# Optimization experiments

Hardware: AMD Instinct MI355X
Metric: run time of the kernel (lower is better)

The kernel has to match this reference:

```python
import jax, jax.numpy as jnp
import numpy as np

B, NQ, NM = 8, 1024, 2048
DIM, HEADS, DHEAD, MLP = 512, 8, 64, 2048
INNER = HEADS * DHEAD
EPS = 1e-5


def layernorm(x, g, b):
    mu = jnp.mean(x, axis=-1, keepdims=True)
    var = jnp.mean(jnp.square(x - mu), axis=-1, keepdims=True)
    return (x - mu) * jax.lax.rsqrt(var + EPS) * g + b


def mha(q_in, k_in, v_in, wq, wk, wv, wo, bo, g, b):
    Bq, Nq, _ = q_in.shape
    Nk = k_in.shape[1]
    q = (q_in @ wq).reshape(Bq, Nq, HEADS, DHEAD)
    k = (k_in @ wk).reshape(Bq, Nk, HEADS, DHEAD)
    v = (v_in @ wv).reshape(Bq, Nk, HEADS, DHEAD)
    scale = DHEAD ** -0.5
    dots = jnp.einsum('bqhd,bkhd->bhqk', q, k) * scale
    attn = jax.nn.softmax(dots, axis=-1)
    out = jnp.einsum('bhqk,bkhd->bqhd', attn, v).reshape(Bq, Nq, INNER)
    out = out @ wo + bo
    return layernorm(out, g, b) + q_in


def ffn(x, w1, b1, w2, b2, g, b):
    h = jax.nn.relu(x @ w1 + b1)
    return layernorm(h @ w2 + b2, g, b) + x


def _mha_params(key, s=0.02):
    ks = jax.random.split(key, 4)
    return dict(
        wq=jax.random.normal(ks[0], (DIM, INNER), jnp.float32) * s,
        wk=jax.random.normal(ks[1], (DIM, INNER), jnp.float32) * s,
        wv=jax.random.normal(ks[2], (DIM, INNER), jnp.float32) * s,
        wo=jax.random.normal(ks[3], (INNER, DIM), jnp.float32) * s,
        bo=jnp.zeros((DIM,), jnp.float32),
        g=jnp.ones((DIM,), jnp.float32),
        b=jnp.zeros((DIM,), jnp.float32),
    )


def _ffn_params(key, s=0.02):
    ks = jax.random.split(key, 2)
    return dict(
        w1=jax.random.normal(ks[0], (DIM, MLP), jnp.float32) * s,
        b1=jnp.zeros((MLP,), jnp.float32),
        w2=jax.random.normal(ks[1], (MLP, DIM), jnp.float32) * s,
        b2=jnp.zeros((DIM,), jnp.float32),
        g=jnp.ones((DIM,), jnp.float32),
        b=jnp.zeros((DIM,), jnp.float32),
    )


def setup_inputs() -> dict:
    key = jax.random.key(0)
    ks = jax.random.split(key, 8)
    inp = {
        'tgt': jax.random.normal(ks[0], (B, NQ, DIM), jnp.float32),
        'memory': jax.random.normal(ks[1], (B, NM, DIM), jnp.float32),
        'pos': jax.random.normal(ks[2], (B, NM, DIM), jnp.float32),
        'query_pos': jax.random.normal(ks[3], (B, NQ, DIM), jnp.float32),
    }
    a0 = _mha_params(ks[4]); f0 = _ffn_params(ks[5])
    a1 = _mha_params(ks[6]); f1 = _ffn_params(ks[7])
    for name, d in (('a0', a0), ('f0', f0), ('a1', a1), ('f1', f1)):
        for k, v in d.items():
            inp[f'{name}_{k}'] = v
    return inp


def reference(tgt, memory, pos, query_pos,
              a0_wq, a0_wk, a0_wv, a0_wo, a0_bo, a0_g, a0_b,
              f0_w1, f0_b1, f0_w2, f0_b2, f0_g, f0_b,
              a1_wq, a1_wk, a1_wv, a1_wo, a1_bo, a1_g, a1_b,
              f1_w1, f1_b1, f1_w2, f1_b2, f1_g, f1_b):
    # self-attention: q=k=tgt+query_pos, v=tgt
    q0 = tgt + query_pos
    x = mha(q0, q0, tgt, a0_wq, a0_wk, a0_wv, a0_wo, a0_bo, a0_g, a0_b)
    x = ffn(x, f0_w1, f0_b1, f0_w2, f0_b2, f0_g, f0_b)
    # cross-attention: q=x+query_pos, k=memory+pos, v=memory
    q = x + query_pos
    k = memory + pos
    x = mha(q, k, memory, a1_wq, a1_wk, a1_wv, a1_wo, a1_bo, a1_g, a1_b)
    x = ffn(x, f1_w1, f1_b1, f1_w2, f1_b2, f1_g, f1_b)
    return x
```

## Files before the change

### kernel.cpp

```cpp
#include <hip/hip_runtime.h>
#include <stdint.h>
#include <stddef.h>

typedef __attribute__((ext_vector_type(8))) short short8;
typedef __attribute__((ext_vector_type(4))) short short4v;
typedef __attribute__((ext_vector_type(4))) float floatx4;

#define DEV __device__ __forceinline__

DEV float bf2f(short s) {
    union { float f; uint32_t u; } v;
    v.u = ((uint32_t)(uint16_t)s) << 16;
    return v.f;
}
DEV short f2bf(float f) {
    union { float f; uint32_t u; } v;
    v.f = f;
    uint32_t u = v.u + 0x7FFFu + ((v.u >> 16) & 1u);
    return (short)(u >> 16);
}
DEV short f2bf_tr(float f) {
    union { float f; uint32_t u; } v;
    v.f = f;
    return (short)(v.u >> 16);
}

template<int BIAS, int RELU, int OUTBF>
__global__ __launch_bounds__(256) void gemm_bt(
    const short* __restrict__ A, const short* __restrict__ Bt,
    const float* __restrict__ bias, void* __restrict__ Cout,
    int M, int N, int K)
{
    __shared__ short Alds[2][128 * 32];
    __shared__ short Blds[2][128 * 32];
    const int tid  = threadIdx.x;
    const int wave = tid >> 6, lane = tid & 63;
    const int g = lane >> 4, li = lane & 15;

    const int gx = gridDim.x;
    int flat = blockIdx.y * gx + blockIdx.x;
    const int nwg = gx * gridDim.y;
    flat = (flat & 7) * (nwg >> 3) + (flat >> 3);
    const long bm = (long)(flat % gx) * 128;
    const long bn = (long)(flat / gx) * 128;

    const int wr = (wave >> 1) * 64;
    const int wc = (wave & 1) * 64;
    const int srow = wave * 32 + (lane >> 2);
    const int scol = (lane & 3) * 8;
    const short* Ap = A + bm * K + (long)srow * K + scol;
    const short* Bp = Bt + bn * K + (long)srow * K + scol;

    auto STAGE = [&](int buf, int k0) {
        __builtin_amdgcn_global_load_lds(
            (const __attribute__((address_space(1))) void*)(Ap + k0),
            (__attribute__((address_space(3))) void*)(&Alds[buf][wave * 1024]), 16, 0, 0);
        __builtin_amdgcn_global_load_lds(
            (const __attribute__((address_space(1))) void*)(Ap + (long)16 * K + k0),
            (__attribute__((address_space(3))) void*)(&Alds[buf][wave * 1024 + 512]), 16, 0, 0);
        __builtin_amdgcn_global_load_lds(
            (const __attribute__((address_space(1))) void*)(Bp + k0),
            (__attribute__((address_space(3))) void*)(&Blds[buf][wave * 1024]), 16, 0, 0);
        __builtin_amdgcn_global_load_lds(
            (const __attribute__((address_space(1))) void*)(Bp + (long)16 * K + k0),
            (__attribute__((address_space(3))) void*)(&Blds[buf][wave * 1024 + 512]), 16, 0, 0);
    };

    floatx4 acc[4][4];
#pragma unroll
    for (int i = 0; i < 4; i++)
#pragma unroll
        for (int j = 0; j < 4; j++) acc[i][j] = (floatx4){0.f, 0.f, 0.f, 0.f};

    STAGE(0, 0);
    __syncthreads();
    int cur = 0;
    for (int k0 = 0; k0 < K; k0 += 32) {
        if (k0 + 32 < K) STAGE(cur ^ 1, k0 + 32);

        short8 af[4], bfr[4];
#pragma unroll
        for (int mi = 0; mi < 4; mi++)
            af[mi] = *(const short8*)(&Alds[cur][(wr + mi * 16 + li) * 32 + g * 8]);
#pragma unroll
        for (int ni = 0; ni < 4; ni++)
            bfr[ni] = *(const short8*)(&Blds[cur][(wc + ni * 16 + li) * 32 + g * 8]);
#pragma unroll
        for (int mi = 0; mi < 4; mi++)
#pragma unroll
            for (int ni = 0; ni < 4; ni++)
                acc[mi][ni] = __builtin_amdgcn_mfma_f32_16x16x32_bf16(
                    af[mi], bfr[ni], acc[mi][ni], 0, 0, 0);

        __syncthreads();
        cur ^= 1;
    }

    float* Cf = (float*)Cout;
    short* Cb = (short*)Cout;
#pragma unroll
    for (int mi = 0; mi < 4; mi++) {
#pragma unroll
        for (int ni = 0; ni < 4; ni++) {
            const long col = bn + wc + ni * 16 + li;
            const float bv = BIAS ? bias[col] : 0.f;
#pragma unroll
            for (int i = 0; i < 4; i++) {
                const long row = bm + wr + mi * 16 + g * 4 + i;
                float v = acc[mi][ni][i] + bv;
                if (RELU) v = fmaxf(v, 0.f);
                if (OUTBF) Cb[row * N + col] = f2bf(v);
                else       Cf[row * N + col] = v;
            }
        }
    }
}

__global__ __launch_bounds__(256) void attn_kernel(
    const short* __restrict__ Qg, const short* __restrict__ Kg,
    const short* __restrict__ VTg, short* __restrict__ Og,
    int NQ, int NK, int ldq, int ldk)
{
    constexpr int LD = 68;
    __shared__ short Klds[32 * LD];
    __shared__ short Vlds[64 * LD];
    __shared__ short Plds[4][16 * LD];

    const int tid = threadIdx.x;
    const int wave = tid >> 6, lane = tid & 63;
    const int g = lane >> 4, li = lane & 15;
    const int b = blockIdx.z, h = blockIdx.y;
    const int q0 = blockIdx.x * 64 + wave * 16;

    const short* qptr = Qg + ((long)(b * NQ + q0 + li) * ldq + h * 64);
    short8 qf[2];
#pragma unroll
    for (int f = 0; f < 2; f++) {
        short8 t = *(const short8*)(qptr + f * 32 + g * 8);
#pragma unroll
        for (int i = 0; i < 8; i++) t[i] = f2bf(bf2f(t[i]) * 0.18033688011112042f);
        qf[f] = t;
    }

    floatx4 acc[4];
#pragma unroll
    for (int s = 0; s < 4; s++) acc[s] = (floatx4){0.f, 0.f, 0.f, 0.f};
    float lsum = 0.f;

    const short* kbase = Kg + (long)b * NK * ldk + h * 64;
    const short* vbase = VTg + ((long)(b * 512 + h * 64)) * NK;
    const int skey = tid >> 3, sdc = (tid & 7) * 8;
    const int svd = tid >> 2, svk = (tid & 3) * 8;

    for (int kt = 0; kt < NK; kt += 32) {
        __syncthreads();
        *(short8*)(Klds + skey * LD + sdc) =
            *(const short8*)(kbase + (long)(kt + skey) * ldk + sdc);
        *(short8*)(Vlds + svd * LD + svk) =
            *(const short8*)(vbase + (long)svd * NK + kt + svk);
        __syncthreads();

        floatx4 sT0 = (floatx4){0.f, 0.f, 0.f, 0.f};
        floatx4 sT1 = (floatx4){0.f, 0.f, 0.f, 0.f};
        {
            short8 k00 = *(const short8*)(Klds + li * LD + g * 8);
            short8 k01 = *(const short8*)(Klds + li * LD + 32 + g * 8);
            short8 k10 = *(const short8*)(Klds + (16 + li) * LD + g * 8);
            short8 k11 = *(const short8*)(Klds + (16 + li) * LD + 32 + g * 8);
            sT0 = __builtin_amdgcn_mfma_f32_16x16x32_bf16(k00, qf[0], sT0, 0, 0, 0);
            sT0 = __builtin_amdgcn_mfma_f32_16x16x32_bf16(k01, qf[1], sT0, 0, 0, 0);
            sT1 = __builtin_amdgcn_mfma_f32_16x16x32_bf16(k10, qf[0], sT1, 0, 0, 0);
            sT1 = __builtin_amdgcn_mfma_f32_16x16x32_bf16(k11, qf[1], sT1, 0, 0, 0);
        }

        const float p0 = exp2f(sT0[0]), p1 = exp2f(sT0[1]);
        const float p2 = exp2f(sT0[2]), p3 = exp2f(sT0[3]);
        const float p4 = exp2f(sT1[0]), p5 = exp2f(sT1[1]);
        const float p6 = exp2f(sT1[2]), p7 = exp2f(sT1[3]);
        lsum += ((p0 + p1) + (p2 + p3)) + ((p4 + p5) + (p6 + p7));

        short4v pw0 = { f2bf_tr(p0), f2bf_tr(p1), f2bf_tr(p2), f2bf_tr(p3) };
        short4v pw1 = { f2bf_tr(p4), f2bf_tr(p5), f2bf_tr(p6), f2bf_tr(p7) };
        *(short4v*)(Plds[wave] + li * LD + g * 4) = pw0;
        *(short4v*)(Plds[wave] + li * LD + 16 + g * 4) = pw1;
        short8 pf = *(const short8*)(Plds[wave] + li * LD + g * 8);

#pragma unroll
        for (int s = 0; s < 4; s++) {
            short8 vf = *(const short8*)(Vlds + (s * 16 + li) * LD + g * 8);
            acc[s] = __builtin_amdgcn_mfma_f32_16x16x32_bf16(vf, pf, acc[s], 0, 0, 0);
        }
    }

    lsum += __shfl_xor(lsum, 16);
    lsum += __shfl_xor(lsum, 32);
    const float inv = 1.f / lsum;
    short* optr = Og + ((long)(b * NQ + q0 + li) * 512 + h * 64);
#pragma unroll
    for (int s = 0; s < 4; s++) {
        short4v o4 = { f2bf(acc[s][0] * inv), f2bf(acc[s][1] * inv),
                       f2bf(acc[s][2] * inv), f2bf(acc[s][3] * inv) };
        *(short4v*)(optr + s * 16 + g * 4) = o4;
    }
}

__global__ __launch_bounds__(256) void add_conv2(
    const float* __restrict__ a, const float* __restrict__ b,
    float* __restrict__ of, short* __restrict__ ob1, short* __restrict__ ob2)
{
    const long i = (long)(blockIdx.x * 256 + threadIdx.x) * 4;
    const float4 va = *(const float4*)(a + i);
    float4 vs = va;
    if (b) {
        const float4 vb = *(const float4*)(b + i);
        vs.x += vb.x; vs.y += vb.y; vs.z += vb.z; vs.w += vb.w;
    }
    if (of) *(float4*)(of + i) = vs;
    short4v o1 = { f2bf(vs.x), f2bf(vs.y), f2bf(vs.z), f2bf(vs.w) };
    *(short4v*)(ob1 + i) = o1;
    if (ob2) {
        short4v o2 = { f2bf(va.x), f2bf(va.y), f2bf(va.z), f2bf(va.w) };
        *(short4v*)(ob2 + i) = o2;
    }
}

__global__ __launch_bounds__(256) void ln_res_kernel(
    const float* __restrict__ X, const float* __restrict__ gam,
    const float* __restrict__ bet, const float* __restrict__ res,
    const float* __restrict__ postadd,
    float* __restrict__ outF, short* __restrict__ outB)
{
    const int row = blockIdx.x * 4 + (threadIdx.x >> 6);
    const int lane = threadIdx.x & 63;
    const long base = (long)row * 512 + lane * 8;
    float x[8];
    *(float4*)(x) = *(const float4*)(X + base);
    *(float4*)(x + 4) = *(const float4*)(X + base + 4);
    float s = x[0] + x[1] + x[2] + x[3] + x[4] + x[5] + x[6] + x[7];
#pragma unroll
    for (int o = 1; o < 64; o <<= 1) s += __shfl_xor(s, o);
    const float mu = s * (1.0f / 512.0f);
    float vs = 0.f;
#pragma unroll
    for (int i = 0; i < 8; i++) { const float d = x[i] - mu; vs += d * d; }
#pragma unroll
    for (int o = 1; o < 64; o <<= 1) vs += __shfl_xor(vs, o);
    const float rs = rsqrtf(vs * (1.0f / 512.0f) + 1e-5f);

    float gv[8], bv[8], rv[8];
    *(float4*)(gv) = *(const float4*)(gam + lane * 8);
    *(float4*)(gv + 4) = *(const float4*)(gam + lane * 8 + 4);
    *(float4*)(bv) = *(const float4*)(bet + lane * 8);
    *(float4*)(bv + 4) = *(const float4*)(bet + lane * 8 + 4);
    *(float4*)(rv) = *(const float4*)(res + base);
    *(float4*)(rv + 4) = *(const float4*)(res + base + 4);

    float y[8];
#pragma unroll
    for (int i = 0; i < 8; i++) y[i] = (x[i] - mu) * rs * gv[i] + bv[i] + rv[i];
    if (postadd) {
        float pv[8];
        *(float4*)(pv) = *(const float4*)(postadd + base);
        *(float4*)(pv + 4) = *(const float4*)(postadd + base + 4);
#pragma unroll
        for (int i = 0; i < 8; i++) y[i] += pv[i];
    }
    *(float4*)(outF + base) = *(float4*)(y);
    *(float4*)(outF + base + 4) = *(float4*)(y + 4);
    if (outB) {
        short8 ob;
#pragma unroll
        for (int i = 0; i < 8; i++) ob[i] = f2bf(y[i]);
        *(short8*)(outB + base) = ob;
    }
}

__global__ __launch_bounds__(256) void wtrans8(
    const float* __restrict__ w0, const float* __restrict__ w1,
    const float* __restrict__ w2, const float* __restrict__ w3,
    const float* __restrict__ w4, const float* __restrict__ w5,
    const float* __restrict__ w6, const float* __restrict__ w7,
    short* __restrict__ o0, short* __restrict__ o1,
    short* __restrict__ o2, short* __restrict__ o3,
    short* __restrict__ o4, short* __restrict__ o5,
    short* __restrict__ o6, short* __restrict__ o7,
    int K, int N)
{
    const float* Ws[8] = {w0, w1, w2, w3, w4, w5, w6, w7};
    short* Os[8] = {o0, o1, o2, o3, o4, o5, o6, o7};
    const float* W = Ws[blockIdx.z];
    short* Wt = Os[blockIdx.z];
    __shared__ short t[32][33];
    const int n0 = blockIdx.x * 32, k0 = blockIdx.y * 32;
    const int tx = threadIdx.x & 31, ty = threadIdx.x >> 5;
    for (int r = ty; r < 32; r += 8)
        t[r][tx] = f2bf(W[(long)(k0 + r) * N + n0 + tx]);
    __syncthreads();
    for (int r = ty; r < 32; r += 8)
        Wt[(long)(n0 + r) * K + k0 + tx] = t[tx][r];
}

__global__ __launch_bounds__(256) void vtrans(
    const short* __restrict__ V, short* __restrict__ VT, int NK)
{
    __shared__ short t[32][33];
    const int b = blockIdx.z;
    const int key0 = blockIdx.x * 32, c0 = blockIdx.y * 32;
    const int tx = threadIdx.x & 31, ty = threadIdx.x >> 5;
    for (int r = ty; r < 32; r += 8)
        t[r][tx] = V[((long)b * NK + key0 + r) * 512 + c0 + tx];
    __syncthreads();
    for (int r = ty; r < 32; r += 8)
        VT[((long)b * 512 + c0 + r) * NK + key0 + tx] = t[tx][r];
}

extern "C" void kernel_launch(void* const* d_in, const int* in_sizes, int n_in,
                              void* d_out, int out_size, void* d_ws, size_t ws_size,
                              hipStream_t stream)
{
    (void)in_sizes; (void)n_in; (void)out_size; (void)ws_size;
    const float* tgt   = (const float*)d_in[0];
    const float* mem   = (const float*)d_in[1];
    const float* pos   = (const float*)d_in[2];
    const float* qpos  = (const float*)d_in[3];
    const float* a0_wq = (const float*)d_in[4];
    const float* a0_wk = (const float*)d_in[5];
    const float* a0_wv = (const float*)d_in[6];
    const float* a0_wo = (const float*)d_in[7];
    const float* a0_bo = (const float*)d_in[8];
    const float* a0_g  = (const float*)d_in[9];
    const float* a0_b  = (const float*)d_in[10];
    const float* f0_w1 = (const float*)d_in[11];
    const float* f0_b1 = (const float*)d_in[12];
    const float* f0_w2 = (const float*)d_in[13];
    const float* f0_b2 = (const float*)d_in[14];
    const float* f0_g  = (const float*)d_in[15];
    const float* f0_b  = (const float*)d_in[16];
    const float* a1_wq = (const float*)d_in[17];
    const float* a1_wk = (const float*)d_in[18];
    const float* a1_wv = (const float*)d_in[19];
    const float* a1_wo = (const float*)d_in[20];
    const float* a1_bo = (const float*)d_in[21];
    const float* a1_g  = (const float*)d_in[22];
    const float* a1_b  = (const float*)d_in[23];
    const float* f1_w1 = (const float*)d_in[24];
    const float* f1_b1 = (const float*)d_in[25];
    const float* f1_w2 = (const float*)d_in[26];
    const float* f1_b2 = (const float*)d_in[27];
    const float* f1_g  = (const float*)d_in[28];
    const float* f1_b  = (const float*)d_in[29];

    const int M1 = 8 * 1024;
    const int M2 = 8 * 2048;
    const size_t MB = 1ull << 20;
    char* ws = (char*)d_ws;

    float* resid = (float*)(ws + 0 * MB);
    float* xf    = (float*)(ws + 16 * MB);
    short* xb    = (short*)(ws + 32 * MB);
    short* wb    = (short*)(ws + 40 * MB);
    short* a0_wqt = wb;            short* a0_wkt = wb + 262144;
    short* a0_wvt = wb + 524288;   short* a0_wot = wb + 786432;
    short* f0_w1t = wb + 1048576;  short* f0_w2t = wb + 2097152;
    short* a1_wqt = wb + 3145728;  short* a1_wkt = wb + 3407872;
    short* a1_wvt = wb + 3670016;  short* a1_wot = wb + 3932160;
    short* f1_w1t = wb + 4194304;  short* f1_w2t = wb + 5242880;
    char* S = ws + 56 * MB;

    wtrans8<<<dim3(16, 16, 8), 256, 0, stream>>>(
        a0_wq, a0_wk, a0_wv, a0_wo, a1_wq, a1_wk, a1_wv, a1_wo,
        a0_wqt, a0_wkt, a0_wvt, a0_wot, a1_wqt, a1_wkt, a1_wvt, a1_wot, 512, 512);
    wtrans8<<<dim3(64, 16, 2), 256, 0, stream>>>(
        f0_w1, f1_w1, nullptr, nullptr, nullptr, nullptr, nullptr, nullptr,
        f0_w1t, f1_w1t, nullptr, nullptr, nullptr, nullptr, nullptr, nullptr, 512, 2048);
    wtrans8<<<dim3(16, 64, 2), 256, 0, stream>>>(
        f0_w2, f1_w2, nullptr, nullptr, nullptr, nullptr, nullptr, nullptr,
        f0_w2t, f1_w2t, nullptr, nullptr, nullptr, nullptr, nullptr, nullptr, 2048, 512);

    short* QKs  = (short*)(S + 0 * MB);
    short* Vs   = (short*)(S + 16 * MB);
    short* VsT  = (short*)(S + 24 * MB);
    short* AOs  = (short*)(S + 32 * MB);
    float* Of   = (float*)(S + 40 * MB);
    short* q0b  = (short*)(S + 56 * MB);
    short* tgtb = (short*)(S + 64 * MB);

    add_conv2<<<4096, 256, 0, stream>>>(tgt, qpos, resid, q0b, tgtb);

    gemm_bt<0,0,1><<<dim3(64, 8), 256, 0, stream>>>(q0b,  a0_wqt, nullptr, QKs, M1, 1024, 512);
    gemm_bt<0,0,1><<<dim3(64, 4), 256, 0, stream>>>(tgtb, a0_wvt, nullptr, Vs, M1, 512, 512);
    vtrans<<<dim3(32, 16, 8), 256, 0, stream>>>(Vs, VsT, 1024);
    attn_kernel<<<dim3(16, 8, 8), 256, 0, stream>>>(QKs, QKs + 512, VsT, AOs,
                                                    1024, 1024, 1024, 1024);
    gemm_bt<1,0,0><<<dim3(64, 4), 256, 0, stream>>>(AOs, a0_wot, a0_bo, Of, M1, 512, 512);
    ln_res_kernel<<<2048, 256, 0, stream>>>(Of, a0_g, a0_b, resid, nullptr, xf, xb);

    short* Hb  = (short*)(S + 0 * MB);
    float* O2f = (float*)(S + 32 * MB);
    short* qcb = (short*)(S + 80 * MB);
    gemm_bt<1,1,1><<<dim3(64, 16), 256, 0, stream>>>(xb, f0_w1t, f0_b1, Hb, M1, 2048, 512);
    gemm_bt<1,0,0><<<dim3(64, 4), 256, 0, stream>>>(Hb, f0_w2t, f0_b2, O2f, M1, 512, 2048);
    ln_res_kernel<<<2048, 256, 0, stream>>>(O2f, f0_g, f0_b, xf, qpos, resid, qcb);

    short* Qc   = (short*)(S + 0 * MB);
    short* Kc   = (short*)(S + 8 * MB);
    short* Vc   = (short*)(S + 24 * MB);
    short* VcT  = (short*)(S + 40 * MB);
    short* AOc  = (short*)(S + 56 * MB);
    float* Ocf  = (float*)(S + 64 * MB);
    short* kcb  = (short*)(S + 88 * MB);
    short* memb = (short*)(S + 104 * MB);

    add_conv2<<<8192, 256, 0, stream>>>(mem, pos, nullptr, kcb, memb);

    gemm_bt<0,0,1><<<dim3(64, 4), 256, 0, stream>>>(qcb,  a1_wqt, nullptr, Qc, M1, 512, 512);
    gemm_bt<0,0,1><<<dim3(128, 4), 256, 0, stream>>>(kcb,  a1_wkt, nullptr, Kc, M2, 512, 512);
    gemm_bt<0,0,1><<<dim3(128, 4), 256, 0, stream>>>(memb, a1_wvt, nullptr, Vc, M2, 512, 512);
    vtrans<<<dim3(64, 16, 8), 256, 0, stream>>>(Vc, VcT, 2048);
    attn_kernel<<<dim3(16, 8, 8), 256, 0, stream>>>(Qc, Kc, VcT, AOc,
                                                    1024, 2048, 512, 512);
    gemm_bt<1,0,0><<<dim3(64, 4), 256, 0, stream>>>(AOc, a1_wot, a1_bo, Ocf, M1, 512, 512);
    ln_res_kernel<<<2048, 256, 0, stream>>>(Ocf, a1_g, a1_b, resid, nullptr, xf, xb);

    short* Hb2  = (short*)(S + 0 * MB);
    float* O3f  = (float*)(S + 32 * MB);
    gemm_bt<1,1,1><<<dim3(64, 16), 256, 0, stream>>>(xb, f1_w1t, f1_b1, Hb2, M1, 2048, 512);
    gemm_bt<1,0,0><<<dim3(64, 4), 256, 0, stream>>>(Hb2, f1_w2t, f1_b2, O3f, M1, 512, 2048);
    ln_res_kernel<<<2048, 256, 0, stream>>>(O3f, f1_g, f1_b, xf, nullptr, (float*)d_out, nullptr);
}
```

Measured before the change: 514.9 us.

## Fuse QKV/KV projections, split-K output GEMMs, prefetch attention tiles

Merges the separate Q/K and V projection GEMMs into a single launch that picks its A operand by output-column range. The N=512 output projections and FFN down-projections now use a two-way split-K, whose partial sums are added inside the layernorm kernel, to fill more workgroups. The attention kernel prefetches the next K/V tile into registers before it is written to LDS, and the P buffer gets a narrower padding stride. This adds an extra fp32 partial buffer write and read for every split-K GEMM and relies on the weight buffers for Q, K and V being laid out contiguously.

```diff
diff --git a/kernel.cpp b/kernel.cpp
--- a/kernel.cpp
+++ b/kernel.cpp
@@ -48,8 +48,8 @@
     const int wc = (wave & 1) * 64;
     const int srow = wave * 32 + (lane >> 2);
     const int scol = (lane & 3) * 8;
-    const short* Ap = A + bm * K + (long)srow * K + scol;
-    const short* Bp = Bt + bn * K + (long)srow * K + scol;
+    const short* Ap = A + (bm + srow) * (long)K + scol;
+    const short* Bp = Bt + (bn + srow) * (long)K + scol;
 
     auto STAGE = [&](int buf, int k0) {
         __builtin_amdgcn_global_load_lds(
@@ -116,15 +116,183 @@
     }
 }
 
+__global__ __launch_bounds__(256) void gemm_bt2(
+    const short* __restrict__ A0, const short* __restrict__ A1,
+    const short* __restrict__ Bt, short* __restrict__ Cout,
+    int M, int N, int K, int nsplit)
+{
+    __shared__ short Alds[2][128 * 32];
+    __shared__ short Blds[2][128 * 32];
+    const int tid  = threadIdx.x;
+    const int wave = tid >> 6, lane = tid & 63;
+    const int g = lane >> 4, li = lane & 15;
+
+    const int gx = gridDim.x;
+    int flat = blockIdx.y * gx + blockIdx.x;
+    const int nwg = gx * gridDim.y;
+    flat = (flat & 7) * (nwg >> 3) + (flat >> 3);
+    const long bm = (long)(flat % gx) * 128;
+    const long bn = (long)(flat / gx) * 128;
+
+    const int wr = (wave >> 1) * 64;
+    const int wc = (wave & 1) * 64;
+    const int srow = wave * 32 + (lane >> 2);
+    const int scol = (lane & 3) * 8;
+    const short* A = (bn < nsplit) ? A0 : A1;
+    const short* Ap = A + (bm + srow) * (long)K + scol;
+    const short* Bp = Bt + (bn + srow) * (long)K + scol;
+
+    auto STAGE = [&](int buf, int k0) {
+        __builtin_amdgcn_global_load_lds(
+            (const __attribute__((address_space(1))) void*)(Ap + k0),
+            (__attribute__((address_space(3))) void*)(&Alds[buf][wave * 1024]), 16, 0, 0);
+        __builtin_amdgcn_global_load_lds(
+            (const __attribute__((address_space(1))) void*)(Ap + (long)16 * K + k0),
+            (__attribute__((address_space(3))) void*)(&Alds[buf][wave * 1024 + 512]), 16, 0, 0);
+        __builtin_amdgcn_global_load_lds(
+            (const __attribute__((address_space(1))) void*)(Bp + k0),
+            (__attribute__((address_space(3))) void*)(&Blds[buf][wave * 1024]), 16, 0, 0);
+        __builtin_amdgcn_global_load_lds(
+            (const __attribute__((address_space(1))) void*)(Bp + (long)16 * K + k0),
+            (__attribute__((address_space(3))) void*)(&Blds[buf][wave * 1024 + 512]), 16, 0, 0);
+    };
+
+    floatx4 acc[4][4];
+#pragma unroll
+    for (int i = 0; i < 4; i++)
+#pragma unroll
+        for (int j = 0; j < 4; j++) acc[i][j] = (floatx4){0.f, 0.f, 0.f, 0.f};
+
+    STAGE(0, 0);
+    __syncthreads();
+    int cur = 0;
+    for (int k0 = 0; k0 < K; k0 += 32) {
+        if (k0 + 32 < K) STAGE(cur ^ 1, k0 + 32);
+        short8 af[4], bfr[4];
+#pragma unroll
+        for (int mi = 0; mi < 4; mi++)
+            af[mi] = *(const short8*)(&Alds[cur][(wr + mi * 16 + li) * 32 + g * 8]);
+#pragma unroll
+        for (int ni = 0; ni < 4; ni++)
+            bfr[ni] = *(const short8*)(&Blds[cur][(wc + ni * 16 + li) * 32 + g * 8]);
+#pragma unroll
+        for (int mi = 0; mi < 4; mi++)
+#pragma unroll
+            for (int ni = 0; ni < 4; ni++)
+                acc[mi][ni] = __builtin_amdgcn_mfma_f32_16x16x32_bf16(
+                    af[mi], bfr[ni], acc[mi][ni], 0, 0, 0);
+        __syncthreads();
+        cur ^= 1;
+    }
+
+#pragma unroll
+    for (int mi = 0; mi < 4; mi++)
+#pragma unroll
+        for (int ni = 0; ni < 4; ni++) {
+            const long col = bn + wc + ni * 16 + li;
+#pragma unroll
+            for (int i = 0; i < 4; i++) {
+                const long row = bm + wr + mi * 16 + g * 4 + i;
+                Cout[row * N + col] = f2bf(acc[mi][ni][i]);
+            }
+        }
+}
+
+template<int BIAS>
+__global__ __launch_bounds__(256) void gemm_bt_sk(
+    const short* __restrict__ A, const short* __restrict__ Bt,
+    const float* __restrict__ bias, float* __restrict__ Cout,
+    int M, int N, int K)
+{
+    __shared__ short Alds[2][128 * 32];
+    __shared__ short Blds[2][128 * 32];
+    const int tid  = threadIdx.x;
+    const int wave = tid >> 6, lane = tid & 63;
+    const int g = lane >> 4, li = lane & 15;
+    const int z = blockIdx.z;
+    const int Kh = K >> 1;
+
+    const int gx = gridDim.x;
+    int flat = blockIdx.y * gx + blockIdx.x;
+    const int nwg = gx * gridDim.y;
+    flat = (flat & 7) * (nwg >> 3) + (flat >> 3);
+    const long bm = (long)(flat % gx) * 128;
+    const long bn = (long)(flat / gx) * 128;
+
+    const int wr = (wave >> 1) * 64;
+    const int wc = (wave & 1) * 64;
+    const int srow = wave * 32 + (lane >> 2);
+    const int scol = (lane & 3) * 8;
+    const short* Ap = A + (bm + srow) * (long)K + scol + (long)z * Kh;
+    const short* Bp = Bt + (bn + srow) * (long)K + scol + (long)z * Kh;
+    float* C = Cout + (long)z * M * N;
+
+    auto STAGE = [&](int buf, int k0) {
+        __builtin_amdgcn_global_load_lds(
+            (const __attribute__((address_space(1))) void*)(Ap + k0),
+            (__attribute__((address_space(3))) void*)(&Alds[buf][wave * 1024]), 16, 0, 0);
+        __builtin_amdgcn_global_load_lds(
+            (const __attribute__((address_space(1))) void*)(Ap + (long)16 * K + k0),
+            (__attribute__((address_space(3))) void*)(&Alds[buf][wave * 1024 + 512]), 16, 0, 0);
+        __builtin_amdgcn_global_load_lds(
+            (const __attribute__((address_space(1))) void*)(Bp + k0),
+            (__attribute__((address_space(3))) void*)(&Blds[buf][wave * 1024]), 16, 0, 0);
+        __builtin_amdgcn_global_load_lds(
+            (const __attribute__((address_space(1))) void*)(Bp + (long)16 * K + k0),
+            (__attribute__((address_space(3))) void*)(&Blds[buf][wave * 1024 + 512]), 16, 0, 0);
+    };
+
+    floatx4 acc[4][4];
+#pragma unroll
+    for (int i = 0; i < 4; i++)
+#pragma unroll
+        for (int j = 0; j < 4; j++) acc[i][j] = (floatx4){0.f, 0.f, 0.f, 0.f};
+
+    STAGE(0, 0);
+    __syncthreads();
+    int cur = 0;
+    for (int k0 = 0; k0 < Kh; k0 += 32) {
+        if (k0 + 32 < Kh) STAGE(cur ^ 1, k0 + 32);
+        short8 af[4], bfr[4];
+#pragma unroll
+        for (int mi = 0; mi < 4; mi++)
+            af[mi] = *(const short8*)(&Alds[cur][(wr + mi * 16 + li) * 32 + g * 8]);
+#pragma unroll
+        for (int ni = 0; ni < 4; ni++)
+            bfr[ni] = *(const short8*)(&Blds[cur][(wc + ni * 16 + li) * 32 + g * 8]);
+#pragma unroll
+        for (int mi = 0; mi < 4; mi++)
+#pragma unroll
+            for (int ni = 0; ni < 4; ni++)
+                acc[mi][ni] = __builtin_amdgcn_mfma_f32_16x16x32_bf16(
+                    af[mi], bfr[ni], acc[mi][ni], 0, 0, 0);
+        __syncthreads();
+        cur ^= 1;
+    }
+
+#pragma unroll
+    for (int mi = 0; mi < 4; mi++)
+#pragma unroll
+        for (int ni = 0; ni < 4; ni++) {
+            const long col = bn + wc + ni * 16 + li;
+            const float bv = (BIAS && z == 0) ? bias[col] : 0.f;
+#pragma unroll
+            for (int i = 0; i < 4; i++) {
+                const long row = bm + wr + mi * 16 + g * 4 + i;
+                C[row * N + col] = acc[mi][ni][i] + bv;
+            }
+        }
+}
+
 __global__ __launch_bounds__(256) void attn_kernel(
     const short* __restrict__ Qg, const short* __restrict__ Kg,
     const short* __restrict__ VTg, short* __restrict__ Og,
     int NQ, int NK, int ldq, int ldk)
 {
-    constexpr int LD = 68;
+    constexpr int LD = 68, LDP = 36;
     __shared__ short Klds[32 * LD];
     __shared__ short Vlds[64 * LD];
-    __shared__ short Plds[4][16 * LD];
+    __shared__ short Plds[4][16 * LDP];
 
     const int tid = threadIdx.x;
     const int wave = tid >> 6, lane = tid & 63;
@@ -147,18 +315,23 @@
     for (int s = 0; s < 4; s++) acc[s] = (floatx4){0.f, 0.f, 0.f, 0.f};
     float lsum = 0.f;
 
-    const short* kbase = Kg + (long)b * NK * ldk + h * 64;
-    const short* vbase = VTg + ((long)(b * 512 + h * 64)) * NK;
     const int skey = tid >> 3, sdc = (tid & 7) * 8;
     const int svd = tid >> 2, svk = (tid & 3) * 8;
+    const short* kp = Kg + (long)b * NK * ldk + h * 64 + (long)skey * ldk + sdc;
+    const short* vp = VTg + ((long)(b * 512 + h * 64 + svd)) * NK + svk;
+
+    short8 kreg = *(const short8*)kp;  kp += (long)32 * ldk;
+    short8 vreg = *(const short8*)vp;  vp += 32;
 
     for (int kt = 0; kt < NK; kt += 32) {
         __syncthreads();
-        *(short8*)(Klds + skey * LD + sdc) =
-            *(const short8*)(kbase + (long)(kt + skey) * ldk + sdc);
-        *(short8*)(Vlds + svd * LD + svk) =
-            *(const short8*)(vbase + (long)svd * NK + kt + svk);
+        *(short8*)(Klds + skey * LD + sdc) = kreg;
+        *(short8*)(Vlds + svd * LD + svk) = vreg;
         __syncthreads();
+        if (kt + 32 < NK) {
+            kreg = *(const short8*)kp;  kp += (long)32 * ldk;
+            vreg = *(const short8*)vp;  vp += 32;
+        }
 
         floatx4 sT0 = (floatx4){0.f, 0.f, 0.f, 0.f};
         floatx4 sT1 = (floatx4){0.f, 0.f, 0.f, 0.f};
@@ -181,9 +354,9 @@
 
         short4v pw0 = { f2bf_tr(p0), f2bf_tr(p1), f2bf_tr(p2), f2bf_tr(p3) };
         short4v pw1 = { f2bf_tr(p4), f2bf_tr(p5), f2bf_tr(p6), f2bf_tr(p7) };
-        *(short4v*)(Plds[wave] + li * LD + g * 4) = pw0;
-        *(short4v*)(Plds[wave] + li * LD + 16 + g * 4) = pw1;
-        short8 pf = *(const short8*)(Plds[wave] + li * LD + g * 8);
+        *(short4v*)(Plds[wave] + li * LDP + g * 4) = pw0;
+        *(short4v*)(Plds[wave] + li * LDP + 16 + g * 4) = pw1;
+        short8 pf = *(const short8*)(Plds[wave] + li * LDP + g * 8);
 
 #pragma unroll
         for (int s = 0; s < 4; s++) {
@@ -225,9 +398,9 @@
 }
 
 __global__ __launch_bounds__(256) void ln_res_kernel(
-    const float* __restrict__ X, const float* __restrict__ gam,
-    const float* __restrict__ bet, const float* __restrict__ res,
-    const float* __restrict__ postadd,
+    const float* __restrict__ X, const float* __restrict__ X2,
+    const float* __restrict__ gam, const float* __restrict__ bet,
+    const float* __restrict__ res, const float* __restrict__ postadd,
     float* __restrict__ outF, short* __restrict__ outB)
 {
     const int row = blockIdx.x * 4 + (threadIdx.x >> 6);
@@ -236,6 +409,13 @@
     float x[8];
     *(float4*)(x) = *(const float4*)(X + base);
     *(float4*)(x + 4) = *(const float4*)(X + base + 4);
+    if (X2) {
+        float x2[8];
+        *(float4*)(x2) = *(const float4*)(X2 + base);
+        *(float4*)(x2 + 4) = *(const float4*)(X2 + base + 4);
+#pragma unroll
+        for (int i = 0; i < 8; i++) x[i] += x2[i];
+    }
     float s = x[0] + x[1] + x[2] + x[3] + x[4] + x[5] + x[6] + x[7];
 #pragma unroll
     for (int o = 1; o < 64; o <<= 1) s += __shfl_xor(s, o);
@@ -301,14 +481,15 @@
 }
 
 __global__ __launch_bounds__(256) void vtrans(
-    const short* __restrict__ V, short* __restrict__ VT, int NK)
+    const short* __restrict__ V, short* __restrict__ VT,
+    int NK, int ldv, int voff)
 {
     __shared__ short t[32][33];
     const int b = blockIdx.z;
     const int key0 = blockIdx.x * 32, c0 = blockIdx.y * 32;
     const int tx = threadIdx.x & 31, ty = threadIdx.x >> 5;
     for (int r = ty; r < 32; r += 8)
-        t[r][tx] = V[((long)b * NK + key0 + r) * 512 + c0 + tx];
+        t[r][tx] = V[((long)b * NK + key0 + r) * ldv + voff + c0 + tx];
     __syncthreads();
     for (int r = ty; r < 32; r += 8)
         VT[((long)b * 512 + c0 + r) * NK + key0 + tx] = t[tx][r];
@@ -377,54 +558,61 @@
         f0_w2, f1_w2, nullptr, nullptr, nullptr, nullptr, nullptr, nullptr,
         f0_w2t, f1_w2t, nullptr, nullptr, nullptr, nullptr, nullptr, nullptr, 2048, 512);
 
-    short* QKs  = (short*)(S + 0 * MB);
-    short* Vs   = (short*)(S + 16 * MB);
+    short* QKVs = (short*)(S + 0 * MB);
     short* VsT  = (short*)(S + 24 * MB);
     short* AOs  = (short*)(S + 32 * MB);
-    float* Of   = (float*)(S + 40 * MB);
-    short* q0b  = (short*)(S + 56 * MB);
-    short* tgtb = (short*)(S + 64 * MB);
+    float* P0a  = (float*)(S + 40 * MB);
+    float* P1a  = (float*)(S + 56 * MB);
+    short* q0b  = (short*)(S + 72 * MB);
+    short* tgtb = (short*)(S + 80 * MB);
 
     add_conv2<<<4096, 256, 0, stream>>>(tgt, qpos, resid, q0b, tgtb);
 
-    gemm_bt<0,0,1><<<dim3(64, 8), 256, 0, stream>>>(q0b,  a0_wqt, nullptr, QKs, M1, 1024, 512);
-    gemm_bt<0,0,1><<<dim3(64, 4), 256, 0, stream>>>(tgtb, a0_wvt, nullptr, Vs, M1, 512, 512);
-    vtrans<<<dim3(32, 16, 8), 256, 0, stream>>>(Vs, VsT, 1024);
-    attn_kernel<<<dim3(16, 8, 8), 256, 0, stream>>>(QKs, QKs + 512, VsT, AOs,
-                                                    1024, 1024, 1024, 1024);
-    gemm_bt<1,0,0><<<dim3(64, 4), 256, 0, stream>>>(AOs, a0_wot, a0_bo, Of, M1, 512, 512);
-    ln_res_kernel<<<2048, 256, 0, stream>>>(Of, a0_g, a0_b, resid, nullptr, xf, xb);
+    gemm_bt2<<<dim3(64, 12), 256, 0, stream>>>(q0b, tgtb, a0_wqt, QKVs,
+                                               M1, 1536, 512, 1024);
+    vtrans<<<dim3(32, 16, 8), 256, 0, stream>>>(QKVs, VsT, 1024, 1536, 1024);
+    attn_kernel<<<dim3(16, 8, 8), 256, 0, stream>>>(QKVs, QKVs + 512, VsT, AOs,
+                                                    1024, 1024, 1536, 1536);
+    gemm_bt_sk<1><<<dim3(64, 4, 2), 256, 0, stream>>>(AOs, a0_wot, a0_bo, P0a,
+                                                      M1, 512, 512);
+    ln_res_kernel<<<2048, 256, 0, stream>>>(P0a, P1a, a0_g, a0_b, resid, nullptr, xf, xb);
 
     short* Hb  = (short*)(S + 0 * MB);
-    float* O2f = (float*)(S + 32 * MB);
-    short* qcb = (short*)(S + 80 * MB);
+    float* P0f = (float*)(S + 32 * MB);
+    float* P1f = (float*)(S + 48 * MB);
+    short* qcb = (short*)(S + 88 * MB);
     gemm_bt<1,1,1><<<dim3(64, 16), 256, 0, stream>>>(xb, f0_w1t, f0_b1, Hb, M1, 2048, 512);
-    gemm_bt<1,0,0><<<dim3(64, 4), 256, 0, stream>>>(Hb, f0_w2t, f0_b2, O2f, M1, 512, 2048);
-    ln_res_kernel<<<2048, 256, 0, stream>>>(O2f, f0_g, f0_b, xf, qpos, resid, qcb);
-
-    short* Qc   = (short*)(S + 0 * MB);
-    short* Kc   = (short*)(S + 8 * MB);
-    short* Vc   = (short*)(S + 24 * MB);
-    short* VcT  = (short*)(S + 40 * MB);
-    short* AOc  = (short*)(S + 56 * MB);
-    float* Ocf  = (float*)(S + 64 * MB);
-    short* kcb  = (short*)(S + 88 * MB);
-    short* memb = (short*)(S + 104 * MB);
+    gemm_bt_sk<1><<<dim3(64, 4, 2), 256, 0, stream>>>(Hb, f0_w2t, f0_b2, P0f,
+                                                      M1, 512, 2048);
+    ln_res_kernel<<<2048, 256, 0, stream>>>(P0f, P1f, f0_g, f0_b, xf, qpos, resid, qcb);
+
+    short* kcb  = (short*)(S + 0 * MB);
+    short* memb = (short*)(S + 16 * MB);
+    short* KVc  = (short*)(S + 32 * MB);
+    float* P0c  = (float*)(S + 32 * MB);
+    float* P1c  = (float*)(S + 48 * MB);
+    short* VcT  = (short*)(S + 64 * MB);
+    short* Qc   = (short*)(S + 80 * MB);
+    short* AOc  = (short*)(S + 96 * MB);
 
     add_conv2<<<8192, 256, 0, stream>>>(mem, pos, nullptr, kcb, memb);
 
-    gemm_bt<0,0,1><<<dim3(64, 4), 256, 0, stream>>>(qcb,  a1_wqt, nullptr, Qc, M1, 512, 512);
-    gemm_bt<0,0,1><<<dim3(128, 4), 256, 0, stream>>>(kcb,  a1_wkt, nullptr, Kc, M2, 512, 512);
-    gemm_bt<0,0,1><<<dim3(128, 4), 256, 0, stream>>>(memb, a1_wvt, nullptr, Vc, M2, 512, 512);
-    vtrans<<<dim3(64, 16, 8), 256, 0, stream>>>(Vc, VcT, 2048);
-    attn_kernel<<<dim3(16, 8, 8), 256, 0, stream>>>(Qc, Kc, VcT, AOc,
-                                                    1024, 2048, 512, 512);
-    gemm_bt<1,0,0><<<dim3(64, 4), 256, 0, stream>>>(AOc, a1_wot, a1_bo, Ocf, M1, 512, 512);
-    ln_res_kernel<<<2048, 256, 0, stream>>>(Ocf, a1_g, a1_b, resid, nullptr, xf, xb);
+    gemm_bt<0,0,1><<<dim3(64, 4), 256, 0, stream>>>(qcb, a1_wqt, nullptr, Qc, M1, 512, 512);
+    gemm_bt2<<<dim3(128, 8), 256, 0, stream>>>(kcb, memb, a1_wkt, KVc,
+                                               M2, 1024, 512, 512);
+    vtrans<<<dim3(64, 16, 8), 256, 0, stream>>>(KVc, VcT, 2048, 1024, 512);
+    attn_kernel<<<dim3(16, 8, 8), 256, 0, stream>>>(Qc, KVc, VcT, AOc,
+                                                    1024, 2048, 512, 1024);
+    gemm_bt_sk<1><<<dim3(64, 4, 2), 256, 0, stream>>>(AOc, a1_wot, a1_bo, P0c,
+                                                      M1, 512, 512);
+    ln_res_kernel<<<2048, 256, 0, stream>>>(P0c, P1c, a1_g, a1_b, resid, nullptr, xf, xb);
 
     short* Hb2  = (short*)(S + 0 * MB);
-    float* O3f  = (float*)(S + 32 * MB);
+    float* P0g  = (float*)(S + 32 * MB);
+    float* P1g  = (float*)(S + 48 * MB);
     gemm_bt<1,1,1><<<dim3(64, 16), 256, 0, stream>>>(xb, f1_w1t, f1_b1, Hb2, M1, 2048, 512);
-    gemm_bt<1,0,0><<<dim3(64, 4), 256, 0, stream>>>(Hb2, f1_w2t, f1_b2, O3f, M1, 512, 2048);
-    ln_res_kernel<<<2048, 256, 0, stream>>>(O3f, f1_g, f1_b, xf, nullptr, (float*)d_out, nullptr);
-}
+    gemm_bt_sk<1><<<dim3(64, 4, 2), 256, 0, stream>>>(Hb2, f1_w2t, f1_b2, P0g,
+                                                      M1, 512, 2048);
+    ln_res_kernel<<<2048, 256, 0, stream>>>(P0g, P1g, f1_g, f1_b, xf, nullptr,
+                                            (float*)d_out, nullptr);
+}
```

Result: faster. 449.2 us (-12.8%).
